# Performance work log

Measured on AMD Instinct MI355X. Metric: run time of the kernel, lower is better.

## Reference

```python
import jax, jax.numpy as jnp
import numpy as np

B, P = 8, 1024
D = 512
BUCKETS = 65536
LS = (8, 7, 6)  # padded ids per patch for ngrams 1,2,3


def setup_inputs() -> dict:
    key = jax.random.key(0)
    ks = jax.random.split(key, 10)
    inp = {}
    for i, L in enumerate(LS):
        inp[f"ids_{i+1}"] = jax.random.randint(ks[i], (B, P, L), 0, BUCKETS, dtype=jnp.int64)
        inp[f"mask_{i+1}"] = jax.random.randint(ks[3 + i], (B, P, L), 0, 2, dtype=jnp.int32).astype(bool)
        inp[f"emb_{i+1}"] = jax.random.normal(ks[6 + i], (BUCKETS, D), dtype=jnp.float32)
    inp["patch_mask"] = jax.random.randint(ks[9], (B, P), 0, 2, dtype=jnp.int32).astype(bool)
    return inp


def reference(ids_1, ids_2, ids_3, mask_1, mask_2, mask_3, patch_mask, emb_1, emb_2, emb_3):
    # For each ngram order: gather [B,P,L,D], zero out padded ids, sum over L.
    out = jnp.zeros((B, P, D), dtype=emb_1.dtype)
    for ids, m, emb in ((ids_1, mask_1, emb_1), (ids_2, mask_2, emb_2), (ids_3, mask_3, emb_3)):
        g = jnp.take(emb, ids, axis=0)               # [B,P,L,D]
        out = out + jnp.where(m[..., None], g, 0).sum(axis=2)
    return jnp.where(patch_mask[..., None], out, 0)
```

## Files before the change

### kernel.cpp

```cpp
#include <hip/hip_runtime.h>


#define D_DIM   512
#define NPATCH  8192
#define NWAVES  (NPATCH * 2)

__device__ __forceinline__ void acc_add(float4& a, const float4 b) {
    a.x += b.x; a.y += b.y; a.z += b.z; a.w += b.w;
}

template <int L>
__device__ __forceinline__ void gather_stage(const int* __restrict__ ids,
                                             const int* __restrict__ mask,
                                             const float* __restrict__ emb,
                                             int foff, float4* __restrict__ t) {
#pragma unroll
    for (int l = 0; l < L; ++l) {
        if (__builtin_amdgcn_readfirstlane(mask[l])) {
            const int sid = __builtin_amdgcn_readfirstlane(ids[l]);
            t[l] = *(const float4*)(emb + (size_t)sid * D_DIM + foff);
        }
    }
}

__global__ __launch_bounds__(256) void patch_embed_kernel(
    const int* __restrict__ ids1, const int* __restrict__ m1, const float* __restrict__ e1,
    const int* __restrict__ ids2, const int* __restrict__ m2, const float* __restrict__ e2,
    const int* __restrict__ ids3, const int* __restrict__ m3, const float* __restrict__ e3,
    const int* __restrict__ pmask, float* __restrict__ out) {
    const int lane = threadIdx.x & 63;
    const int gw   = (blockIdx.x << 2) | (threadIdx.x >> 6);
    const int patch = __builtin_amdgcn_readfirstlane(gw >> 1);
    const int foff  = ((gw & 1) << 8) | (lane << 2);

    float4 t[21];
#pragma unroll
    for (int i = 0; i < 21; ++i) t[i] = make_float4(0.f, 0.f, 0.f, 0.f);

    if (__builtin_amdgcn_readfirstlane(pmask[patch])) {
        gather_stage<8>(ids1 + patch * 8, m1 + patch * 8, e1, foff, t);
        gather_stage<7>(ids2 + patch * 7, m2 + patch * 7, e2, foff, t + 8);
        gather_stage<6>(ids3 + patch * 6, m3 + patch * 6, e3, foff, t + 15);
    }

    float4 acc = t[0];
#pragma unroll
    for (int i = 1; i < 21; ++i) acc_add(acc, t[i]);

    *(float4*)(out + (size_t)patch * D_DIM + foff) = acc;
}

extern "C" void kernel_launch(void* const* d_in, const int* in_sizes, int n_in,
                              void* d_out, int out_size, void* d_ws, size_t ws_size,
                              hipStream_t stream) {
    const int*   ids1  = (const int*)d_in[0];
    const int*   m1    = (const int*)d_in[1];
    const float* e1    = (const float*)d_in[2];
    const int*   ids2  = (const int*)d_in[3];
    const int*   m2    = (const int*)d_in[4];
    const float* e2    = (const float*)d_in[5];
    const int*   ids3  = (const int*)d_in[6];
    const int*   m3    = (const int*)d_in[7];
    const float* e3    = (const float*)d_in[8];
    const int*   pmask = (const int*)d_in[9];
    float* out = (float*)d_out;

    dim3 grid(NWAVES / 4);
    dim3 block(256);
    patch_embed_kernel<<<grid, block, 0, stream>>>(ids1, m1, e1, ids2, m2, e2,
                                                   ids3, m3, e3, pmask, out);
}
```

Baseline: 307.2 us.

## Split patches across four waves with float2 loads and lane-loaded ids

Each patch is now handled by four waves, each covering 128 features with float2 loads, instead of two waves covering 256 features with float4. Ids and masks are loaded once as vectors across lanes and broadcast with readlane, replacing per-id scalar loads. Masked-out ids now read row 0 unconditionally and are multiplied by a 0/1 scale rather than branched around. This raises parallelism and removes divergent branches, but issues narrower loads, launches twice as many waves, and fetches rows even for masked slots.

New measurement: 309.4 us. About the same (+0.7%).

```diff
diff --git a/kernel.cpp b/kernel.cpp
--- a/kernel.cpp
+++ b/kernel.cpp
@@ -3,23 +3,20 @@
 
 #define D_DIM   512
 #define NPATCH  8192
-#define NWAVES  (NPATCH * 2)
-
-__device__ __forceinline__ void acc_add(float4& a, const float4 b) {
-    a.x += b.x; a.y += b.y; a.z += b.z; a.w += b.w;
-}
 
 template <int L>
-__device__ __forceinline__ void gather_stage(const int* __restrict__ ids,
-                                             const int* __restrict__ mask,
-                                             const float* __restrict__ emb,
-                                             int foff, float4* __restrict__ t) {
+__device__ __forceinline__ void stage(int vi, int vm,
+                                      const float* __restrict__ emb,
+                                      int foff,
+                                      float2* __restrict__ t,
+                                      float* __restrict__ sc) {
 #pragma unroll
     for (int l = 0; l < L; ++l) {
-        if (__builtin_amdgcn_readfirstlane(mask[l])) {
-            const int sid = __builtin_amdgcn_readfirstlane(ids[l]);
-            t[l] = *(const float4*)(emb + (size_t)sid * D_DIM + foff);
-        }
+        const int sm  = __builtin_amdgcn_readlane(vm, l);
+        int       sid = __builtin_amdgcn_readlane(vi, l);
+        sid   = (sm && (unsigned)sid < 65536u) ? sid : 0;
+        sc[l] = sm ? 1.0f : 0.0f;
+        t[l]  = *(const float2*)(emb + (size_t)sid * D_DIM + foff);
     }
 }
 
@@ -28,26 +25,35 @@
     const int* __restrict__ ids2, const int* __restrict__ m2, const float* __restrict__ e2,
     const int* __restrict__ ids3, const int* __restrict__ m3, const float* __restrict__ e3,
     const int* __restrict__ pmask, float* __restrict__ out) {
-    const int lane = threadIdx.x & 63;
-    const int gw   = (blockIdx.x << 2) | (threadIdx.x >> 6);
-    const int patch = __builtin_amdgcn_readfirstlane(gw >> 1);
-    const int foff  = ((gw & 1) << 8) | (lane << 2);
+    const int lane  = threadIdx.x & 63;
+    const int gw    = (blockIdx.x << 2) | (threadIdx.x >> 6);
+    const int patch = __builtin_amdgcn_readfirstlane(gw >> 2);
+    const int foff  = ((gw & 3) << 7) | (lane << 1);
 
-    float4 t[21];
-#pragma unroll
-    for (int i = 0; i < 21; ++i) t[i] = make_float4(0.f, 0.f, 0.f, 0.f);
+    float2 acc = make_float2(0.f, 0.f);
 
     if (__builtin_amdgcn_readfirstlane(pmask[patch])) {
-        gather_stage<8>(ids1 + patch * 8, m1 + patch * 8, e1, foff, t);
-        gather_stage<7>(ids2 + patch * 7, m2 + patch * 7, e2, foff, t + 8);
-        gather_stage<6>(ids3 + patch * 6, m3 + patch * 6, e3, foff, t + 15);
+        const int vi1 = ids1[patch * 8 + ((lane < 8) ? lane : 7)];
+        const int vm1 = m1  [patch * 8 + ((lane < 8) ? lane : 7)];
+        const int vi2 = ids2[patch * 7 + ((lane < 7) ? lane : 6)];
+        const int vm2 = m2  [patch * 7 + ((lane < 7) ? lane : 6)];
+        const int vi3 = ids3[patch * 6 + ((lane < 6) ? lane : 5)];
+        const int vm3 = m3  [patch * 6 + ((lane < 6) ? lane : 5)];
+
+        float2 t[21];
+        float  sc[21];
+        stage<8>(vi1, vm1, e1, foff, t,      sc);
+        stage<7>(vi2, vm2, e2, foff, t + 8,  sc + 8);
+        stage<6>(vi3, vm3, e3, foff, t + 15, sc + 15);
+
+#pragma unroll
+        for (int l = 0; l < 21; ++l) {
+            acc.x += sc[l] * t[l].x;
+            acc.y += sc[l] * t[l].y;
+        }
     }
 
-    float4 acc = t[0];
-#pragma unroll
-    for (int i = 1; i < 21; ++i) acc_add(acc, t[i]);
-
-    *(float4*)(out + (size_t)patch * D_DIM + foff) = acc;
+    *(float2*)(out + (size_t)patch * D_DIM + foff) = acc;
 }
 
 extern "C" void kernel_launch(void* const* d_in, const int* in_sizes, int n_in,
@@ -65,7 +71,7 @@
     const int*   pmask = (const int*)d_in[9];
     float* out = (float*)d_out;
 
-    dim3 grid(NWAVES / 4);
+    dim3 grid(NPATCH);
     dim3 block(256);
     patch_embed_kernel<<<grid, block, 0, stream>>>(ids1, m1, e1, ids2, m2, e2,
                                                    ids3, m3, e3, pmask, out);
```
